# Kernel optimization log

Measured on AMD Instinct MI355X. Metric: run time of the kernel, lower is better.

## Reference

```python
import jax, jax.numpy as jnp
import numpy as np

E = 500000
D = 128  # dim_hidden


def _glorot(key, fan_in, fan_out):
    lim = np.sqrt(1.0 / fan_in)
    return jax.random.uniform(key, (fan_in, fan_out), jnp.float32, -lim, lim)


def setup_inputs() -> dict:
    key = jax.random.key(0)
    ks = jax.random.split(key, 9)
    return {
        "src": jax.random.normal(ks[0], (E, D), jnp.float32),
        "dest": jax.random.normal(ks[1], (E, D), jnp.float32),
        "edge_attr": jax.random.normal(ks[2], (E, D), jnp.float32),
        # MLP [3D, D, D, D]: Linear(3D,D), SiLU, Linear(D,D), SiLU, Linear(D,D)
        "W0": _glorot(ks[3], 3 * D, D),
        "b0": jnp.zeros((D,), jnp.float32),
        "W1": _glorot(ks[4], D, D),
        "b1": jnp.zeros((D,), jnp.float32),
        "W2": _glorot(ks[5], D, D),
        "b2": jnp.zeros((D,), jnp.float32),
    }


def reference(src, dest, edge_attr, W0, b0, W1, b1, W2, b2):
    # out = cat([edge_attr, src, dest], dim=1) -> [E, 3D]
    x = jnp.concatenate([edge_attr, src, dest], axis=1)
    h = jax.nn.silu(x @ W0 + b0)      # [E, D]
    h = jax.nn.silu(h @ W1 + b1)      # [E, D]
    out = h @ W2 + b2                 # [E, D] (no activation after last layer)
    return out
```

## Files before the change

kernel.cpp:

```cpp
#include <hip/hip_runtime.h>
#include <hip/hip_bf16.h>

typedef __bf16 bf16;
typedef bf16 bf16x8 __attribute__((ext_vector_type(8)));
typedef bf16 bf16x4 __attribute__((ext_vector_type(4)));
typedef float floatx4 __attribute__((ext_vector_type(4)));

#define LDS_STRIDE 136

__global__ void repack_weights(const float* __restrict__ W0,
                               const float* __restrict__ W1,
                               const float* __restrict__ W2,
                               bf16* __restrict__ Wt0,
                               bf16* __restrict__ Wt1,
                               bf16* __restrict__ Wt2) {
    int t = blockIdx.x * blockDim.x + threadIdx.x;
    const int S0 = 384 * 128, S1 = 128 * 128;
    if (t < S0) {
        int k = t >> 7, n = t & 127;
        Wt0[n * 384 + k] = (bf16)W0[t];
    } else if (t < S0 + S1) {
        int i = t - S0;
        int k = i >> 7, n = i & 127;
        Wt1[n * 128 + k] = (bf16)W1[i];
    } else if (t < S0 + 2 * S1) {
        int i = t - S0 - S1;
        int k = i >> 7, n = i & 127;
        Wt2[n * 128 + k] = (bf16)W2[i];
    }
}

__global__ void edge_mlp(const float* __restrict__ src,
                         const float* __restrict__ dest,
                         const float* __restrict__ edge_attr,
                         const bf16* __restrict__ Wt0,
                         const bf16* __restrict__ Wt1,
                         const bf16* __restrict__ Wt2,
                         const float* __restrict__ b0,
                         const float* __restrict__ b1,
                         const float* __restrict__ b2,
                         float* __restrict__ out,
                         int E) {
    __shared__ bf16 Ax[128 * LDS_STRIDE];

    const int tid  = threadIdx.x;
    const int wave = tid >> 6;
    const int lane = tid & 63;
    const int wm   = wave >> 1;
    const int wn   = wave & 1;
    const int l15  = lane & 15;
    const int quad = lane >> 4;

    const long row0 = (long)blockIdx.x * 128;

    const floatx4 zero4 = {0.f, 0.f, 0.f, 0.f};
    floatx4 acc[4][4];
#pragma unroll
    for (int i = 0; i < 4; ++i)
#pragma unroll
        for (int j = 0; j < 4; ++j) acc[i][j] = zero4;

    auto gemm_tile = [&](const bf16* __restrict__ Wt, int wstride, int kofs) {
#pragma unroll
        for (int ks = 0; ks < 4; ++ks) {
            const int kk = ks * 32 + quad * 8;
            bf16x8 a[4], b[4];
#pragma unroll
            for (int i = 0; i < 4; ++i) {
                int r = wm * 64 + i * 16 + l15;
                a[i] = *(const bf16x8*)&Ax[r * LDS_STRIDE + kk];
            }
#pragma unroll
            for (int j = 0; j < 4; ++j) {
                int n = wn * 64 + j * 16 + l15;
                b[j] = *(const bf16x8*)(Wt + n * wstride + kofs + kk);
            }
#pragma unroll
            for (int i = 0; i < 4; ++i)
#pragma unroll
                for (int j = 0; j < 4; ++j)
                    acc[i][j] = __builtin_amdgcn_mfma_f32_16x16x32_bf16(
                        a[i], b[j], acc[i][j], 0, 0, 0);
        }
    };

    auto epilogue_silu = [&](const float* __restrict__ bias) {
#pragma unroll
        for (int j = 0; j < 4; ++j) {
            int n = wn * 64 + j * 16 + l15;
            float bv = bias[n];
#pragma unroll
            for (int i = 0; i < 4; ++i) {
                int rb = wm * 64 + i * 16 + quad * 4;
#pragma unroll
                for (int q = 0; q < 4; ++q) {
                    float x = acc[i][j][q] + bv;
                    float s = x / (1.f + __expf(-x));
                    Ax[(rb + q) * LDS_STRIDE + n] = (bf16)s;
                }
                acc[i][j] = zero4;
            }
        }
    };

    const float* chunk_ptr[3] = {edge_attr, src, dest};
    for (int c = 0; c < 3; ++c) {
        const float* __restrict__ xin = chunk_ptr[c];
#pragma unroll
        for (int it = 0; it < 16; ++it) {
            int r  = it * 8 + (tid >> 5);
            int c4 = (tid & 31) * 4;
            long gr = row0 + r;
            float4 v;
            if (gr < E) v = *(const float4*)(xin + gr * 128 + c4);
            else        v = make_float4(0.f, 0.f, 0.f, 0.f);
            bf16x4 bv;
            bv[0] = (bf16)v.x; bv[1] = (bf16)v.y;
            bv[2] = (bf16)v.z; bv[3] = (bf16)v.w;
            *(bf16x4*)&Ax[r * LDS_STRIDE + c4] = bv;
        }
        __syncthreads();
        gemm_tile(Wt0, 384, c * 128);
        __syncthreads();
    }
    epilogue_silu(b0);
    __syncthreads();

    gemm_tile(Wt1, 128, 0);
    __syncthreads();
    epilogue_silu(b1);
    __syncthreads();

    gemm_tile(Wt2, 128, 0);
#pragma unroll
    for (int j = 0; j < 4; ++j) {
        int n = wn * 64 + j * 16 + l15;
        float bv = b2[n];
#pragma unroll
        for (int i = 0; i < 4; ++i) {
            int rb = wm * 64 + i * 16 + quad * 4;
#pragma unroll
            for (int q = 0; q < 4; ++q) {
                long gr = row0 + rb + q;
                if (gr < E) out[gr * 128 + n] = acc[i][j][q] + bv;
            }
        }
    }
}

extern "C" void kernel_launch(void* const* d_in, const int* in_sizes, int n_in,
                              void* d_out, int out_size, void* d_ws, size_t ws_size,
                              hipStream_t stream) {
    const float* src       = (const float*)d_in[0];
    const float* dest      = (const float*)d_in[1];
    const float* edge_attr = (const float*)d_in[2];
    const float* W0        = (const float*)d_in[3];
    const float* b0        = (const float*)d_in[4];
    const float* W1        = (const float*)d_in[5];
    const float* b1        = (const float*)d_in[6];
    const float* W2        = (const float*)d_in[7];
    const float* b2        = (const float*)d_in[8];
    float*       out       = (float*)d_out;

    const int E = in_sizes[0] / 128;

    bf16* Wt0 = (bf16*)d_ws;
    bf16* Wt1 = Wt0 + 128 * 384;
    bf16* Wt2 = Wt1 + 128 * 128;

    repack_weights<<<(384 * 128 + 2 * 128 * 128 + 255) / 256, 256, 0, stream>>>(
        W0, W1, W2, Wt0, Wt1, Wt2);

    const int nblk = (E + 127) / 128;
    edge_mlp<<<nblk, 256, 0, stream>>>(src, dest, edge_attr, Wt0, Wt1, Wt2,
                                       b0, b1, b2, out, E);
}
```

Before: 1.004 ms.

## Make MLP kernel persistent with double-buffered register prefetch over 64-row tiles

Converts the edge MLP kernel into a persistent grid-stride loop over 64-row tiles, capped at 2048 blocks. It uses two LDS buffers and prefetches the next input chunk into registers while the MFMA work for the current chunk runs, so global loads overlap with compute. Tile height drops from 128 to 64 rows, which shrinks the accumulators and LDS use, and launch bounds are set to allow 4 blocks per CU. Biases are hoisted out of the loop into registers. The cost is that each weight fragment is reused across fewer rows, so there is more weight traffic per output row.

```diff
diff --git a/kernel.cpp b/kernel.cpp
--- a/kernel.cpp
+++ b/kernel.cpp
@@ -7,6 +7,8 @@
 typedef float floatx4 __attribute__((ext_vector_type(4)));
 
 #define LDS_STRIDE 136
+#define TILE_ROWS  64
+#define TILE_ELEMS (TILE_ROWS * LDS_STRIDE)
 
 __global__ void repack_weights(const float* __restrict__ W0,
                                const float* __restrict__ W1,
@@ -30,18 +32,19 @@
     }
 }
 
-__global__ void edge_mlp(const float* __restrict__ src,
-                         const float* __restrict__ dest,
-                         const float* __restrict__ edge_attr,
-                         const bf16* __restrict__ Wt0,
-                         const bf16* __restrict__ Wt1,
-                         const bf16* __restrict__ Wt2,
-                         const float* __restrict__ b0,
-                         const float* __restrict__ b1,
-                         const float* __restrict__ b2,
-                         float* __restrict__ out,
-                         int E) {
-    __shared__ bf16 Ax[128 * LDS_STRIDE];
+__global__ __launch_bounds__(256, 4) void edge_mlp(
+        const float* __restrict__ src,
+        const float* __restrict__ dest,
+        const float* __restrict__ edge_attr,
+        const bf16* __restrict__ Wt0,
+        const bf16* __restrict__ Wt1,
+        const bf16* __restrict__ Wt2,
+        const float* __restrict__ b0,
+        const float* __restrict__ b1,
+        const float* __restrict__ b2,
+        float* __restrict__ out,
+        int E) {
+    __shared__ bf16 lds[2 * TILE_ELEMS];
 
     const int tid  = threadIdx.x;
     const int wave = tid >> 6;
@@ -51,32 +54,65 @@
     const int l15  = lane & 15;
     const int quad = lane >> 4;
 
-    const long row0 = (long)blockIdx.x * 128;
+    const long ntiles   = ((long)E + TILE_ROWS - 1) / TILE_ROWS;
+    const long stride_t = gridDim.x;
+
+    float bv0[4], bv1[4], bv2[4];
+#pragma unroll
+    for (int j = 0; j < 4; ++j) {
+        int n = wn * 64 + j * 16 + l15;
+        bv0[j] = b0[n]; bv1[j] = b1[n]; bv2[j] = b2[n];
+    }
+
+    const int sr = tid >> 5;
+    const int sc = (tid & 31) * 4;
+
+    float4 pf[8];
+
+    auto pf_load = [&](const float* __restrict__ xin, long t) {
+        const long row0 = t * TILE_ROWS;
+        if (row0 + TILE_ROWS <= (long)E) {
+#pragma unroll
+            for (int it = 0; it < 8; ++it)
+                pf[it] = *(const float4*)(xin + (row0 + it * 8 + sr) * 128 + sc);
+        } else {
+#pragma unroll
+            for (int it = 0; it < 8; ++it) {
+                long gr = row0 + it * 8 + sr;
+                if (gr >= 0 && gr < (long)E) pf[it] = *(const float4*)(xin + gr * 128 + sc);
+                else                         pf[it] = make_float4(0.f, 0.f, 0.f, 0.f);
+            }
+        }
+    };
+
+    auto pf_store = [&](bf16* __restrict__ B) {
+#pragma unroll
+        for (int it = 0; it < 8; ++it) {
+            int r = it * 8 + sr;
+            bf16x4 bv;
+            bv[0] = (bf16)pf[it].x; bv[1] = (bf16)pf[it].y;
+            bv[2] = (bf16)pf[it].z; bv[3] = (bf16)pf[it].w;
+            *(bf16x4*)&B[r * LDS_STRIDE + sc] = bv;
+        }
+    };
 
     const floatx4 zero4 = {0.f, 0.f, 0.f, 0.f};
-    floatx4 acc[4][4];
-#pragma unroll
-    for (int i = 0; i < 4; ++i)
-#pragma unroll
-        for (int j = 0; j < 4; ++j) acc[i][j] = zero4;
-
-    auto gemm_tile = [&](const bf16* __restrict__ Wt, int wstride, int kofs) {
+    floatx4 acc[2][4];
+
+    auto gemm_tile = [&](const bf16* __restrict__ B, const bf16* __restrict__ Wt,
+                         int wstride, int kofs) {
 #pragma unroll
         for (int ks = 0; ks < 4; ++ks) {
             const int kk = ks * 32 + quad * 8;
-            bf16x8 a[4], b[4];
-#pragma unroll
-            for (int i = 0; i < 4; ++i) {
-                int r = wm * 64 + i * 16 + l15;
-                a[i] = *(const bf16x8*)&Ax[r * LDS_STRIDE + kk];
-            }
-#pragma unroll
-            for (int j = 0; j < 4; ++j) {
-                int n = wn * 64 + j * 16 + l15;
-                b[j] = *(const bf16x8*)(Wt + n * wstride + kofs + kk);
-            }
-#pragma unroll
-            for (int i = 0; i < 4; ++i)
+            bf16x8 a[2], b[4];
+#pragma unroll
+            for (int i = 0; i < 2; ++i)
+                a[i] = *(const bf16x8*)&B[(wm * 32 + i * 16 + l15) * LDS_STRIDE + kk];
+#pragma unroll
+            for (int j = 0; j < 4; ++j)
+                b[j] = *(const bf16x8*)(Wt + (wn * 64 + j * 16 + l15) * wstride + kofs + kk);
+#pragma unroll
+            for (int i = 0; i < 2; ++i)
 #pragma unroll
                 for (int j = 0; j < 4; ++j)
                     acc[i][j] = __builtin_amdgcn_mfma_f32_16x16x32_bf16(
@@ -84,67 +120,92 @@
         }
     };
 
-    auto epilogue_silu = [&](const float* __restrict__ bias) {
+    auto epilogue_silu = [&](bf16* __restrict__ H, const float* bv) {
 #pragma unroll
         for (int j = 0; j < 4; ++j) {
             int n = wn * 64 + j * 16 + l15;
-            float bv = bias[n];
-#pragma unroll
-            for (int i = 0; i < 4; ++i) {
-                int rb = wm * 64 + i * 16 + quad * 4;
+#pragma unroll
+            for (int i = 0; i < 2; ++i) {
+                int rb = wm * 32 + i * 16 + quad * 4;
 #pragma unroll
                 for (int q = 0; q < 4; ++q) {
-                    float x = acc[i][j][q] + bv;
+                    float x = acc[i][j][q] + bv[j];
                     float s = x / (1.f + __expf(-x));
-                    Ax[(rb + q) * LDS_STRIDE + n] = (bf16)s;
+                    H[(rb + q) * LDS_STRIDE + n] = (bf16)s;
                 }
                 acc[i][j] = zero4;
             }
         }
     };
 
-    const float* chunk_ptr[3] = {edge_attr, src, dest};
-    for (int c = 0; c < 3; ++c) {
-        const float* __restrict__ xin = chunk_ptr[c];
-#pragma unroll
-        for (int it = 0; it < 16; ++it) {
-            int r  = it * 8 + (tid >> 5);
-            int c4 = (tid & 31) * 4;
-            long gr = row0 + r;
-            float4 v;
-            if (gr < E) v = *(const float4*)(xin + gr * 128 + c4);
-            else        v = make_float4(0.f, 0.f, 0.f, 0.f);
-            bf16x4 bv;
-            bv[0] = (bf16)v.x; bv[1] = (bf16)v.y;
-            bv[2] = (bf16)v.z; bv[3] = (bf16)v.w;
-            *(bf16x4*)&Ax[r * LDS_STRIDE + c4] = bv;
-        }
-        __syncthreads();
-        gemm_tile(Wt0, 384, c * 128);
-        __syncthreads();
-    }
-    epilogue_silu(b0);
+    long t = blockIdx.x;
+    if (t >= ntiles) return;
+
+    pf_load(edge_attr, t);
+    pf_store(lds);
+    int sel = 0;
     __syncthreads();
 
-    gemm_tile(Wt1, 128, 0);
-    __syncthreads();
-    epilogue_silu(b1);
-    __syncthreads();
-
-    gemm_tile(Wt2, 128, 0);
-#pragma unroll
-    for (int j = 0; j < 4; ++j) {
-        int n = wn * 64 + j * 16 + l15;
-        float bv = b2[n];
-#pragma unroll
-        for (int i = 0; i < 4; ++i) {
-            int rb = wm * 64 + i * 16 + quad * 4;
-#pragma unroll
-            for (int q = 0; q < 4; ++q) {
-                long gr = row0 + rb + q;
-                if (gr < E) out[gr * 128 + n] = acc[i][j][q] + bv;
-            }
-        }
+    for (; t < ntiles; t += stride_t) {
+        bf16* BB = lds + sel * TILE_ELEMS;
+        bf16* BA = lds + (sel ^ 1) * TILE_ELEMS;
+
+#pragma unroll
+        for (int i = 0; i < 2; ++i)
+#pragma unroll
+            for (int j = 0; j < 4; ++j) acc[i][j] = zero4;
+
+        pf_load(src, t);
+        gemm_tile(BB, Wt0, 384, 0);
+        pf_store(BA);
+        pf_load(dest, t);
+        __syncthreads();
+
+        gemm_tile(BA, Wt0, 384, 128);
+        pf_store(BB);
+        pf_load(edge_attr, t + stride_t);
+        __syncthreads();
+
+        gemm_tile(BB, Wt0, 384, 256);
+        epilogue_silu(BA, bv0);
+        __syncthreads();
+
+        gemm_tile(BA, Wt1, 128, 0);
+        epilogue_silu(BB, bv1);
+        __syncthreads();
+
+        gemm_tile(BB, Wt2, 128, 0);
+        const long row0 = t * TILE_ROWS;
+        if (row0 + TILE_ROWS <= (long)E) {
+#pragma unroll
+            for (int j = 0; j < 4; ++j) {
+                int n = wn * 64 + j * 16 + l15;
+#pragma unroll
+                for (int i = 0; i < 2; ++i) {
+                    int rb = wm * 32 + i * 16 + quad * 4;
+#pragma unroll
+                    for (int q = 0; q < 4; ++q)
+                        out[(row0 + rb + q) * 128 + n] = acc[i][j][q] + bv2[j];
+                }
+            }
+        } else {
+#pragma unroll
+            for (int j = 0; j < 4; ++j) {
+                int n = wn * 64 + j * 16 + l15;
+#pragma unroll
+                for (int i = 0; i < 2; ++i) {
+                    int rb = wm * 32 + i * 16 + quad * 4;
+#pragma unroll
+                    for (int q = 0; q < 4; ++q) {
+                        long gr = row0 + rb + q;
+                        if (gr < (long)E) out[gr * 128 + n] = acc[i][j][q] + bv2[j];
+                    }
+                }
+            }
+        }
+        pf_store(BA);
+        __syncthreads();
+        sel ^= 1;
     }
 }
 
@@ -163,6 +224,7 @@
     float*       out       = (float*)d_out;
 
     const int E = in_sizes[0] / 128;
+    if (E <= 0) return;
 
     bf16* Wt0 = (bf16*)d_ws;
     bf16* Wt1 = Wt0 + 128 * 384;
@@ -171,7 +233,8 @@
     repack_weights<<<(384 * 128 + 2 * 128 * 128 + 255) / 256, 256, 0, stream>>>(
         W0, W1, W2, Wt0, Wt1, Wt2);
 
-    const int nblk = (E + 127) / 128;
+    const long ntiles = ((long)E + TILE_ROWS - 1) / TILE_ROWS;
+    const int  nblk   = (int)(ntiles < 2048 ? ntiles : 2048);
     edge_mlp<<<nblk, 256, 0, stream>>>(src, dest, edge_attr, Wt0, Wt1, Wt2,
                                        b0, b1, b2, out, E);
 }
```

After: 1.439 ms. 43.3% more time.
